# Optimization experiments

Measured on AMD Instinct MI355X. Metric: run time of the kernel, lower is better.

Reference implementation:

```python
import jax, jax.numpy as jnp
import numpy as np

NUM_EMBEDDINGS = 4096
EMBEDDING_DIM = 4096
COMMITMENT_COST = 0.25


def setup_inputs() -> dict:
    key = jax.random.key(0)
    k_in, k_cb = jax.random.split(key)
    inputs = jax.random.normal(k_in, (16, 512, EMBEDDING_DIM), dtype=jnp.float32)
    bound = 1.0 / NUM_EMBEDDINGS
    codebook = jax.random.uniform(
        k_cb, (NUM_EMBEDDINGS, EMBEDDING_DIM), dtype=jnp.float32,
        minval=-bound, maxval=bound)
    return {"inputs": inputs, "codebook": codebook}


def reference(inputs, codebook):
    B, K, D = inputs.shape
    flat = inputs.reshape(-1, D)  # [N, D], N = B*K
    distances = (
        jnp.sum(flat * flat, axis=1, keepdims=True)
        + jnp.sum(codebook * codebook, axis=1)
        - 2.0 * jnp.matmul(flat, codebook.T)
    )  # [N, num_embeddings]
    encoding_indices = jnp.argmin(distances, axis=1)  # [N]
    quantized = codebook[encoding_indices].reshape(B, K, D)

    e_latent_loss = jnp.mean((jax.lax.stop_gradient(quantized) - inputs) ** 2)
    q_latent_loss = jnp.mean((quantized - jax.lax.stop_gradient(inputs)) ** 2)
    loss = q_latent_loss + COMMITMENT_COST * e_latent_loss

    # straight-through estimator
    quantized_st = inputs + jax.lax.stop_gradient(quantized - inputs)

    # perplexity: codebook usage entropy (scatter one-hot == bincount)
    N = flat.shape[0]
    counts = jnp.zeros((NUM_EMBEDDINGS,), jnp.float32).at[encoding_indices].add(1.0)
    avg_probs = counts / N
    perplexity = jnp.exp(-jnp.sum(avg_probs * jnp.log(avg_probs + 1e-10)))

    return quantized_st, loss, perplexity
```

## Files before the change

### kernel.cpp

```cpp
#include <hip/hip_runtime.h>
#include <hip/hip_bf16.h>
#include <stdint.h>

typedef unsigned int u32;
typedef unsigned char u8;
typedef unsigned long long u64;
typedef __attribute__((ext_vector_type(8))) int i32x8;
typedef __attribute__((ext_vector_type(4))) int i32x4;
typedef __attribute__((ext_vector_type(4))) float f32x4;

#define NROWS 8192
#define NCODES 4096
#define DIM 4096
#define BK 128
#define KSTEPS (DIM / BK)
#define BM 256
#define BN 256

#define OFF_A      0UL
#define OFF_B      33554432UL
#define OFF_NORMS  50331648UL
#define OFF_RN     50348032UL
#define OFF_AMIN   50380800UL
#define OFF_COUNTS 50446336UL

__device__ __forceinline__ void stage16(const void* g, void* l) {
  __builtin_amdgcn_global_load_lds(
      (const __attribute__((address_space(1))) u32*)g,
      (__attribute__((address_space(3))) u32*)l, 16, 0, 0);
}

__device__ __forceinline__ u32 f2fp8(float f) {
  u32 u = __float_as_uint(f);
  u32 sign = (u >> 24) & 0x80u;
  u32 mag = u & 0x7FFFFFFFu;
  if (mag > 0x43E00000u) mag = 0x43E00000u;
  u32 b;
  if (mag < 0x3C800000u) {
    b = (u32)__float2int_rn(__uint_as_float(mag) * 512.0f);
  } else {
    u32 m = mag + 0x7FFFFu + ((mag >> 20) & 1u);
    u32 e = (m >> 23) - 127u;
    b = (((e + 7u) << 3) | ((m >> 20) & 7u)) & 0x7Fu;
  }
  return sign | b;
}

__device__ __forceinline__ u32 pack4(float4 v) {
  return f2fp8(v.x) | (f2fp8(v.y) << 8) | (f2fp8(v.z) << 16) | (f2fp8(v.w) << 24);
}

__device__ __forceinline__ float waveRed(float s) {
#pragma unroll
  for (int off = 32; off > 0; off >>= 1) s += __shfl_down(s, off);
  return s;
}

__device__ __forceinline__ i32x8 comb(i32x4 lo, i32x4 hi) {
  i32x8 r;
  r[0] = lo[0]; r[1] = lo[1]; r[2] = lo[2]; r[3] = lo[3];
  r[4] = hi[0]; r[5] = hi[1]; r[6] = hi[2]; r[7] = hi[3];
  return r;
}

__global__ void k_init(u64* __restrict__ amin, u32* __restrict__ counts) {
  int t = blockIdx.x * 256 + threadIdx.x;
  if (t < NROWS) amin[t] = ~0ULL;
  if (t < NCODES) counts[t] = 0u;
}

__global__ void k_cvtA(const float4* __restrict__ in, u32* __restrict__ outA,
                       float* __restrict__ rn) {
  int r = blockIdx.x;
  const float4* src = in + (size_t)r * (DIM / 4);
  u32* dst = outA + (size_t)r * (DIM / 4);
  float s = 0.0f;
#pragma unroll
  for (int q = 0; q < 4; ++q) {
    int j = q * 256 + threadIdx.x;
    float4 v = src[j];
    s += v.x * v.x + v.y * v.y + v.z * v.z + v.w * v.w;
    dst[j] = pack4(v);
  }
  s = waveRed(s);
  __shared__ float red[4];
  int wid = threadIdx.x >> 6, lane = threadIdx.x & 63;
  if (lane == 0) red[wid] = s;
  __syncthreads();
  if (threadIdx.x == 0) rn[r] = red[0] + red[1] + red[2] + red[3];
}

__global__ void k_cvtB(const float* __restrict__ cb, u32* __restrict__ Bb,
                       float* __restrict__ norms) {
  int row = blockIdx.x;
  const float4* src = (const float4*)(cb + (size_t)row * DIM);
  u32* dst = Bb + (size_t)row * (DIM / 4);
  float s = 0.0f;
#pragma unroll
  for (int q = 0; q < 4; ++q) {
    int j = q * 256 + threadIdx.x;
    float4 v = src[j];
    s += v.x * v.x + v.y * v.y + v.z * v.z + v.w * v.w;
    float4 sv;
    sv.x = v.x * 4096.0f; sv.y = v.y * 4096.0f;
    sv.z = v.z * 4096.0f; sv.w = v.w * 4096.0f;
    dst[j] = pack4(sv);
  }
  s = waveRed(s);
  __shared__ float red[4];
  int wid = threadIdx.x >> 6, lane = threadIdx.x & 63;
  if (lane == 0) red[wid] = s;
  __syncthreads();
  if (threadIdx.x == 0) norms[row] = red[0] + red[1] + red[2] + red[3];
}

__launch_bounds__(512, 1)
__global__ void k_gemm_argmin(const u8* __restrict__ A,
                              const u8* __restrict__ B,
                              const float* __restrict__ norms,
                              u64* __restrict__ amin) {
  __shared__ u8 As[2][BM * BK];
  __shared__ u8 Bs[2][BN * BK];

  const int lb = blockIdx.y * gridDim.x + blockIdx.x;
  const int swz = (lb & 7) * 64 + (lb >> 3);
  const int bm = swz & 31;
  const int bn = swz >> 5;

  const int tid = threadIdx.x;
  const int w = tid >> 6;
  const int lane = tid & 63;
  const int wr = w >> 2, wc = w & 3;
  const int g = lane >> 4, c = lane & 15;

  const size_t rowA0 = (size_t)bm * BM;
  const size_t rowB0 = (size_t)bn * BN;

  const int colb = (((tid & 7) ^ ((tid >> 3) & 7)) << 4);
  const int srow = tid >> 3;
  const u8* gA = A + rowA0 * DIM + colb;
  const u8* gB = B + rowB0 * DIM + colb;

  const int colo = (((2 * g) ^ (c & 7)) << 4);
  const int cohi = (((2 * g + 1) ^ (c & 7)) << 4);

  f32x4 acc[8][4] = {};

#define STAGE(buf, kt_)                                                   \
  {                                                                       \
    _Pragma("unroll") for (int j = 0; j < 4; ++j) {                       \
      int o = j * 8192 + tid * 16;                                        \
      int row = j * 64 + srow;                                            \
      stage16(gA + (size_t)row * DIM + (size_t)(kt_)*BK,                  \
              (char*)As[buf] + o);                                        \
      stage16(gB + (size_t)row * DIM + (size_t)(kt_)*BK,                  \
              (char*)Bs[buf] + o);                                        \
    }                                                                     \
  }

#define COMPUTE(buf)                                                      \
  {                                                                       \
    i32x8 bv[4];                                                          \
    _Pragma("unroll") for (int n = 0; n < 4; ++n) {                       \
      int rown = (wc * 64 + n * 16 + c) * BK;                             \
      bv[n] = comb(*(const i32x4*)&Bs[buf][rown + colo],                  \
                   *(const i32x4*)&Bs[buf][rown + cohi]);                 \
    }                                                                     \
    _Pragma("unroll") for (int m = 0; m < 8; ++m) {                       \
      int rowm = (wr * 128 + m * 16 + c) * BK;                            \
      i32x8 af = comb(*(const i32x4*)&As[buf][rowm + colo],               \
                      *(const i32x4*)&As[buf][rowm + cohi]);              \
      _Pragma("unroll") for (int n = 0; n < 4; ++n)                       \
          acc[m][n] = __builtin_amdgcn_mfma_scale_f32_16x16x128_f8f6f4(   \
              af, bv[n], acc[m][n], 0, 0, 0, 0x7F7F7F7F, 0, 0x7F7F7F7F);  \
    }                                                                     \
  }

#define WAIT8_BAR()                                          \
  asm volatile("s_waitcnt vmcnt(8)" ::: "memory");           \
  __builtin_amdgcn_s_barrier();                              \
  __builtin_amdgcn_sched_barrier(0);

#define BAR()                                                \
  __builtin_amdgcn_s_barrier();                              \
  __builtin_amdgcn_sched_barrier(0);

  STAGE(0, 0);

#pragma unroll 1
  for (int kt2 = 0; kt2 < 15; ++kt2) {
    STAGE(1, 2 * kt2 + 1);
    WAIT8_BAR();
    COMPUTE(0);
    BAR();
    STAGE(0, 2 * kt2 + 2);
    WAIT8_BAR();
    COMPUTE(1);
    BAR();
  }
  STAGE(1, 31);
  WAIT8_BAR();
  COMPUTE(0);
  asm volatile("s_waitcnt vmcnt(0)" ::: "memory");
  __builtin_amdgcn_s_barrier();
  __builtin_amdgcn_sched_barrier(0);
  COMPUTE(1);

#undef STAGE
#undef COMPUTE
#undef WAIT8_BAR
#undef BAR

  const int rowBase = bm * BM + wr * 128;
  const int colBase = bn * BN + wc * 64;
  float nr[4];
#pragma unroll
  for (int n = 0; n < 4; ++n) nr[n] = norms[colBase + n * 16 + c];

#pragma unroll
  for (int m = 0; m < 8; ++m) {
#pragma unroll
    for (int j = 0; j < 4; ++j) {
      u64 key = ~0ULL;
#pragma unroll
      for (int n = 0; n < 4; ++n) {
        float d = nr[n] - acc[m][n][j] * 4.8828125e-4f;
        u32 u = __float_as_uint(d);
        u = (u & 0x80000000u) ? ~u : (u | 0x80000000u);
        u64 k2 = ((u64)u << 32) | (u32)(colBase + n * 16 + c);
        if (k2 < key) key = k2;
      }
#pragma unroll
      for (int off = 1; off < 16; off <<= 1) {
        u64 o = __shfl_xor(key, off);
        if (o < key) key = o;
      }
      if (c == 0) atomicMin(&amin[rowBase + m * 16 + g * 4 + j], key);
    }
  }
}

__global__ void k_out(const float4* __restrict__ cb, const u64* __restrict__ amin,
                      float4* __restrict__ out, u32* __restrict__ counts) {
  int r = blockIdx.x;
  u32 idx = (u32)(amin[r] & 0xFFFFFFFFu);
  if (threadIdx.x == 0) atomicAdd(&counts[idx], 1u);
  const float4* crow = cb + (size_t)idx * (DIM / 4);
  float4* orow = out + (size_t)r * (DIM / 4);
#pragma unroll
  for (int q = 0; q < 4; ++q) {
    int j = q * 256 + threadIdx.x;
    orow[j] = crow[j];
  }
}

__global__ void k_final(const u32* __restrict__ counts, const u64* __restrict__ amin,
                        const float* __restrict__ rn, float* __restrict__ out) {
  float acc = 0.0f;
  for (int r = threadIdx.x; r < NROWS; r += 256) {
    u32 u = (u32)(amin[r] >> 32);
    u32 b = (u & 0x80000000u) ? (u & 0x7FFFFFFFu) : ~u;
    acc += __uint_as_float(b) + rn[r];
  }
  float ent = 0.0f;
  for (int i = threadIdx.x; i < NCODES; i += 256) {
    float p = (float)counts[i] * (1.0f / (float)NROWS);
    ent -= p * logf(p + 1e-10f);
  }
  acc = waveRed(acc);
  ent = waveRed(ent);
  __shared__ float ra[4], re[4];
  int wid = threadIdx.x >> 6, lane = threadIdx.x & 63;
  if (lane == 0) { ra[wid] = acc; re[wid] = ent; }
  __syncthreads();
  if (threadIdx.x == 0) {
    float sse = ra[0] + ra[1] + ra[2] + ra[3];
    float e = re[0] + re[1] + re[2] + re[3];
    out[(size_t)NROWS * DIM] = 1.25f * sse * (1.0f / (float)((size_t)NROWS * DIM));
    out[(size_t)NROWS * DIM + 1] = expf(e);
  }
}

extern "C" void kernel_launch(void* const* d_in, const int* in_sizes, int n_in,
                              void* d_out, int out_size, void* d_ws, size_t ws_size,
                              hipStream_t stream) {
  const float* d_inputs = (const float*)d_in[0];
  const float* d_cb = (const float*)d_in[1];
  float* out = (float*)d_out;
  char* ws = (char*)d_ws;

  u8* A = (u8*)(ws + OFF_A);
  u8* B = (u8*)(ws + OFF_B);
  float* norms = (float*)(ws + OFF_NORMS);
  float* rn = (float*)(ws + OFF_RN);
  u64* amin = (u64*)(ws + OFF_AMIN);
  u32* counts = (u32*)(ws + OFF_COUNTS);

  k_init<<<32, 256, 0, stream>>>(amin, counts);
  k_cvtA<<<NROWS, 256, 0, stream>>>((const float4*)d_inputs, (u32*)A, rn);
  k_cvtB<<<NCODES, 256, 0, stream>>>(d_cb, (u32*)B, norms);
  dim3 grid(NROWS / BM, NCODES / BN);
  k_gemm_argmin<<<grid, 512, 0, stream>>>(A, B, norms, amin);
  k_out<<<NROWS, 256, 0, stream>>>((const float4*)d_cb, amin, (float4*)out, counts);
  k_final<<<1, 256, 0, stream>>>(counts, amin, rn, out);
}
```

Baseline: 270.9 us.

## Fold init into conversion kernels, drop block swizzle and post-compute sched barriers

```diff
diff --git a/kernel.cpp b/kernel.cpp
--- a/kernel.cpp
+++ b/kernel.cpp
@@ -63,15 +63,10 @@
   return r;
 }
 
-__global__ void k_init(u64* __restrict__ amin, u32* __restrict__ counts) {
-  int t = blockIdx.x * 256 + threadIdx.x;
-  if (t < NROWS) amin[t] = ~0ULL;
-  if (t < NCODES) counts[t] = 0u;
-}
-
 __global__ void k_cvtA(const float4* __restrict__ in, u32* __restrict__ outA,
-                       float* __restrict__ rn) {
+                       float* __restrict__ rn, u64* __restrict__ amin) {
   int r = blockIdx.x;
+  if (threadIdx.x == 64) amin[r] = ~0ULL;
   const float4* src = in + (size_t)r * (DIM / 4);
   u32* dst = outA + (size_t)r * (DIM / 4);
   float s = 0.0f;
@@ -91,8 +86,9 @@
 }
 
 __global__ void k_cvtB(const float* __restrict__ cb, u32* __restrict__ Bb,
-                       float* __restrict__ norms) {
+                       float* __restrict__ norms, u32* __restrict__ counts) {
   int row = blockIdx.x;
+  if (threadIdx.x == 64) counts[row] = 0u;
   const float4* src = (const float4*)(cb + (size_t)row * DIM);
   u32* dst = Bb + (size_t)row * (DIM / 4);
   float s = 0.0f;
@@ -122,10 +118,8 @@
   __shared__ u8 As[2][BM * BK];
   __shared__ u8 Bs[2][BN * BK];
 
-  const int lb = blockIdx.y * gridDim.x + blockIdx.x;
-  const int swz = (lb & 7) * 64 + (lb >> 3);
-  const int bm = swz & 31;
-  const int bn = swz >> 5;
+  const int bm = blockIdx.x;
+  const int bn = blockIdx.y;
 
   const int tid = threadIdx.x;
   const int w = tid >> 6;
@@ -142,7 +136,6 @@
   const u8* gB = B + rowB0 * DIM + colb;
 
   const int colo = (((2 * g) ^ (c & 7)) << 4);
-  const int cohi = (((2 * g + 1) ^ (c & 7)) << 4);
 
   f32x4 acc[8][4] = {};
 
@@ -164,12 +157,12 @@
     _Pragma("unroll") for (int n = 0; n < 4; ++n) {                       \
       int rown = (wc * 64 + n * 16 + c) * BK;                             \
       bv[n] = comb(*(const i32x4*)&Bs[buf][rown + colo],                  \
-                   *(const i32x4*)&Bs[buf][rown + cohi]);                 \
+                   *(const i32x4*)&Bs[buf][rown + (colo ^ 16)]);          \
     }                                                                     \
     _Pragma("unroll") for (int m = 0; m < 8; ++m) {                       \
       int rowm = (wr * 128 + m * 16 + c) * BK;                            \
       i32x8 af = comb(*(const i32x4*)&As[buf][rowm + colo],               \
-                      *(const i32x4*)&As[buf][rowm + cohi]);              \
+                      *(const i32x4*)&As[buf][rowm + (colo ^ 16)]);       \
       _Pragma("unroll") for (int n = 0; n < 4; ++n)                       \
           acc[m][n] = __builtin_amdgcn_mfma_scale_f32_16x16x128_f8f6f4(   \
               af, bv[n], acc[m][n], 0, 0, 0, 0x7F7F7F7F, 0, 0x7F7F7F7F);  \
@@ -178,10 +171,6 @@
 
 #define WAIT8_BAR()                                          \
   asm volatile("s_waitcnt vmcnt(8)" ::: "memory");           \
-  __builtin_amdgcn_s_barrier();                              \
-  __builtin_amdgcn_sched_barrier(0);
-
-#define BAR()                                                \
   __builtin_amdgcn_s_barrier();                              \
   __builtin_amdgcn_sched_barrier(0);
 
@@ -192,11 +181,11 @@
     STAGE(1, 2 * kt2 + 1);
     WAIT8_BAR();
     COMPUTE(0);
-    BAR();
+    __builtin_amdgcn_s_barrier();
     STAGE(0, 2 * kt2 + 2);
     WAIT8_BAR();
     COMPUTE(1);
-    BAR();
+    __builtin_amdgcn_s_barrier();
   }
   STAGE(1, 31);
   WAIT8_BAR();
@@ -209,7 +198,6 @@
 #undef STAGE
 #undef COMPUTE
 #undef WAIT8_BAR
-#undef BAR
 
   const int rowBase = bm * BM + wr * 128;
   const int colBase = bn * BN + wc * 64;
@@ -296,9 +284,8 @@
   u64* amin = (u64*)(ws + OFF_AMIN);
   u32* counts = (u32*)(ws + OFF_COUNTS);
 
-  k_init<<<32, 256, 0, stream>>>(amin, counts);
-  k_cvtA<<<NROWS, 256, 0, stream>>>((const float4*)d_inputs, (u32*)A, rn);
-  k_cvtB<<<NCODES, 256, 0, stream>>>(d_cb, (u32*)B, norms);
+  k_cvtA<<<NROWS, 256, 0, stream>>>((const float4*)d_inputs, (u32*)A, rn, amin);
+  k_cvtB<<<NCODES, 256, 0, stream>>>(d_cb, (u32*)B, norms, counts);
   dim3 grid(NROWS / BM, NCODES / BN);
   k_gemm_argmin<<<grid, 512, 0, stream>>>(A, B, norms, amin);
   k_out<<<NROWS, 256, 0, stream>>>((const float4*)d_cb, amin, (float4*)out, counts);
```

New measurement: 267.4 us. About the same (-1.3%).
